# Kernel optimization log

Measured on AMD Instinct MI355X. Metric: run time of the kernel, lower is better.

The kernel has to match this reference:

```python
import jax, jax.numpy as jnp
import numpy as np
import math

B_, CIN, CH, COUT, H_, W_ = 4, 96, 96, 96, 48, 48
DSTATE, DTRANK = 16, math.ceil(CH / 16)
DI = 2 * CH


def conv2d(x, w, b=None, groups=1):
    # x: NCHW, w: OIHW, 'same' padding for odd kernels
    p = (w.shape[-1] - 1) // 2
    y = jax.lax.conv_general_dilated(x, w, (1, 1), [(p, p), (p, p)],
                                     dimension_numbers=('NCHW', 'OIHW', 'NCHW'),
                                     feature_group_count=groups)
    return y if b is None else y + b[None, :, None, None]


def layernorm_last(x, g, b, eps=1e-5):
    mu = x.mean(-1, keepdims=True)
    v = jnp.mean((x - mu) ** 2, -1, keepdims=True)
    return (x - mu) * jax.lax.rsqrt(v + eps) * g + b


def selective_scan(u, delta, A, Bs, Cs, D):
    # u, delta: (B,K,Di,L); A: (K,Di,N); Bs, Cs: (B,K,N,L); D: (K,Di)
    dt = jnp.moveaxis(delta, -1, 0)  # (L,B,K,Di)
    ut = jnp.moveaxis(u, -1, 0)
    Bt = jnp.moveaxis(Bs, -1, 0)     # (L,B,K,N)
    Ct = jnp.moveaxis(Cs, -1, 0)
    N = A.shape[-1]

    def step(h, inp):
        d, uu, bb, cc = inp
        # h: (B,K,Di,N)
        h = h * jnp.exp(d[..., None] * A) + (d * uu)[..., None] * bb[:, :, None, :]
        y = jnp.einsum('bkdn,bkn->bkd', h, cc)
        return h, y

    step = jax.checkpoint(step)
    h0 = jnp.zeros(u.shape[:3] + (N,), u.dtype)
    _, ys = jax.lax.scan(step, h0, (dt, ut, Bt, Ct))
    return jnp.moveaxis(ys, 0, -1) + u * D[None, :, :, None]


def ss2d(x, in_w, cw, cb, xpw, dtw, dtb, A_log, Dp, ong, onb, ow):
    # x: (B,H,W,C) -> (B,H,W,C)
    B, H, W, C = x.shape
    Di = in_w.shape[0] // 2
    xi, z = jnp.split(x @ in_w.T, 2, -1)
    xc = jax.nn.silu(conv2d(jnp.transpose(xi, (0, 3, 1, 2)), cw, cb, groups=Di))
    L = H * W
    xf = xc.reshape(B, Di, L)
    xwh = jnp.transpose(xc, (0, 1, 3, 2)).reshape(B, Di, L)
    xh = jnp.stack([xf, xwh], 1)                      # (B,2,Di,L)
    xs = jnp.concatenate([xh, jnp.flip(xh, -1)], 1)   # (B,4,Di,L) 4-direction cross-scan
    xdbl = jnp.einsum('bkdl,kcd->bkcl', xs, xpw)
    R = dtw.shape[-1]
    N = A_log.shape[-1]
    dts, Bs, Cs = jnp.split(xdbl, [R, R + N], axis=2)
    delta = jax.nn.softplus(jnp.einsum('bkrl,kdr->bkdl', dts, dtw) + dtb[None, :, :, None])
    A = -jnp.exp(A_log.reshape(4, Di, N))
    oy = selective_scan(xs, delta, A, Bs, Cs, Dp.reshape(4, Di))  # (B,4,Di,L)
    inv = jnp.flip(oy[:, 2:4], -1)
    why = jnp.transpose(oy[:, 1].reshape(B, Di, W, H), (0, 1, 3, 2)).reshape(B, Di, L)
    invwhy = jnp.transpose(inv[:, 1].reshape(B, Di, W, H), (0, 1, 3, 2)).reshape(B, Di, L)
    y = oy[:, 0] + inv[:, 0] + why + invwhy           # (B,Di,L)
    y = layernorm_last(jnp.transpose(y, (0, 2, 1)).reshape(B, H, W, Di), ong, onb)
    return (y * jax.nn.silu(z)) @ ow.T


def crm(x, s1, s2, gw, gb, p1, p2):
    C = x.shape[1]
    uc = C // 2
    up = conv2d(x[:, :uc], s1)
    low = conv2d(x[:, uc:], s2)
    Y1 = conv2d(up, gw, gb, groups=2) + conv2d(up, p1)
    Y2 = jnp.concatenate([conv2d(low, p2), low], 1)
    out = jnp.concatenate([Y1, Y2], 1)                # (B,2C,H,W)
    out = jax.nn.softmax(out.mean((2, 3), keepdims=True), axis=1) * out
    o1, o2 = jnp.split(out, 2, 1)
    return o1 + o2


def _forward(x, conv1_w, conv1_b, bn_g, bn_b, lin_w, lin_b, dw1_w, dw1_b, dw2_w, dw2_b, ag1_w, ag1_b, ag2_w, ag2_b, ln_g, ln_b, sq1_w, sq2_w, gwc_w, gwc_b, pwc1_w, pwc2_w, fin_w, fin_b, ss_in_w, ss_conv_w, ss_conv_b, ss_xproj_w, ss_dt_w, ss_dt_b, ss_Alog, ss_D, ss_outn_g, ss_outn_b, ss_out_w):
    C = conv1_w.shape[0]
    # conv1x1 + BatchNorm(eval: running mean 0, var 1) + ReLU
    h = conv2d(x, conv1_w, conv1_b)
    h = jax.nn.relu(h * (bn_g * jax.lax.rsqrt(jnp.float32(1.0 + 1e-5)))[None, :, None, None] + bn_b[None, :, None, None])
    # token-wise linear over channels
    t = jnp.transpose(h, (0, 2, 3, 1)) @ lin_w.T + lin_b
    h = jnp.transpose(t, (0, 3, 1, 2))
    # branch 1: DWConv -> SiLU -> SS2D
    x1 = jax.nn.silu(conv2d(h, dw1_w, dw1_b, groups=C))
    x1 = ss2d(jnp.transpose(x1, (0, 2, 3, 1)), ss_in_w, ss_conv_w, ss_conv_b,
              ss_xproj_w, ss_dt_w, ss_dt_b, ss_Alog, ss_D, ss_outn_g, ss_outn_b, ss_out_w)
    x1 = jnp.transpose(x1, (0, 3, 1, 2))
    # branch 2: DWConv -> SiLU -> AttentionGate modulation
    x2 = jax.nn.silu(conv2d(h, dw2_w, dw2_b, groups=C))
    g = jax.nn.sigmoid(conv2d(jax.nn.relu(conv2d(x2, ag1_w, ag1_b)), ag2_w, ag2_b))
    y = x1 + x2 * g
    # per-pixel channel LayerNorm
    mu = y.mean(1, keepdims=True)
    v = jnp.mean((y - mu) ** 2, 1, keepdims=True)
    y = (y - mu) * jax.lax.rsqrt(v + 1e-5) * ln_g[None, :, None, None] + ln_b[None, :, None, None]
    y = crm(y, sq1_w, sq2_w, gwc_w, gwc_b, pwc1_w, pwc2_w)
    out = jnp.transpose(y, (0, 2, 3, 1)) @ fin_w.T + fin_b
    return jnp.transpose(out, (0, 3, 1, 2))


def setup_inputs():
    key = jax.random.key(0)

    def rnd(i, shape, s=0.02):
        return (jax.random.normal(jax.random.fold_in(key, i), shape) * s).astype(jnp.float32)

    CH2, N, R = CH // 2, DSTATE, DTRANK
    inp = dict(
        x=jax.random.normal(jax.random.fold_in(key, 0), (B_, CIN, H_, W_), jnp.float32),
        conv1_w=rnd(1, (CH, CIN, 1, 1)), conv1_b=jnp.zeros((CH,), jnp.float32),
        bn_g=jnp.ones((CH,), jnp.float32), bn_b=jnp.zeros((CH,), jnp.float32),
        lin_w=rnd(2, (CH, CH)), lin_b=jnp.zeros((CH,), jnp.float32),
        dw1_w=rnd(3, (CH, 1, 3, 3)), dw1_b=jnp.zeros((CH,), jnp.float32),
        dw2_w=rnd(4, (CH, 1, 3, 3)), dw2_b=jnp.zeros((CH,), jnp.float32),
        ag1_w=rnd(5, (CH2, CH, 1, 1)), ag1_b=jnp.zeros((CH2,), jnp.float32),
        ag2_w=rnd(6, (CH, CH2, 1, 1)), ag2_b=jnp.zeros((CH,), jnp.float32),
        ln_g=jnp.ones((CH,), jnp.float32), ln_b=jnp.zeros((CH,), jnp.float32),
        sq1_w=rnd(7, (CH // 4, CH2, 1, 1)), sq2_w=rnd(8, (CH // 4, CH2, 1, 1)),
        gwc_w=rnd(9, (CH, CH // 8, 3, 3)), gwc_b=jnp.zeros((CH,), jnp.float32),
        pwc1_w=rnd(10, (CH, CH // 4, 1, 1)), pwc2_w=rnd(11, (CH - CH // 4, CH // 4, 1, 1)),
        fin_w=rnd(12, (COUT, CH)), fin_b=jnp.zeros((COUT,), jnp.float32),
        ss_in_w=rnd(13, (2 * DI, CH)),
        ss_conv_w=rnd(14, (DI, 1, 3, 3)), ss_conv_b=jnp.zeros((DI,), jnp.float32),
        ss_xproj_w=rnd(15, (4, R + 2 * N, DI)),
        ss_dt_w=rnd(16, (4, DI, R), R ** -0.5),
    )
    dt = jnp.exp(jax.random.uniform(jax.random.fold_in(key, 17), (4, DI)) *
                 (math.log(0.1) - math.log(0.001)) + math.log(0.001))
    inp['ss_dt_b'] = (dt + jnp.log(-jnp.expm1(-dt))).astype(jnp.float32)
    inp['ss_Alog'] = jnp.tile(jnp.log(jnp.arange(1, DSTATE + 1, dtype=jnp.float32))[None, :], (4 * DI, 1))
    inp['ss_D'] = jnp.ones((4 * DI,), jnp.float32)
    inp['ss_outn_g'] = jnp.ones((DI,), jnp.float32)
    inp['ss_outn_b'] = jnp.zeros((DI,), jnp.float32)
    inp['ss_out_w'] = rnd(18, (CH, DI))
    return inp


def reference(x, conv1_w, conv1_b, bn_g, bn_b, lin_w, lin_b, dw1_w, dw1_b, dw2_w, dw2_b, ag1_w, ag1_b, ag2_w, ag2_b, ln_g, ln_b, sq1_w, sq2_w, gwc_w, gwc_b, pwc1_w, pwc2_w, fin_w, fin_b, ss_in_w, ss_conv_w, ss_conv_b, ss_xproj_w, ss_dt_w, ss_dt_b, ss_Alog, ss_D, ss_outn_g, ss_outn_b, ss_out_w):
    return _forward(x, conv1_w, conv1_b, bn_g, bn_b, lin_w, lin_b, dw1_w, dw1_b, dw2_w, dw2_b, ag1_w, ag1_b, ag2_w, ag2_b, ln_g, ln_b, sq1_w, sq2_w, gwc_w, gwc_b, pwc1_w, pwc2_w, fin_w, fin_b, ss_in_w, ss_conv_w, ss_conv_b, ss_xproj_w, ss_dt_w, ss_dt_b, ss_Alog, ss_D, ss_outn_g, ss_outn_b, ss_out_w)
```

## Files before the change

### kernel.cpp

```cpp
#include <hip/hip_runtime.h>
#include <hip/hip_bf16.h>

#define Bn   4
#define CHn  96
#define Hh   48
#define Ww   48
#define Ll   2304
#define Pp   9216
#define DIn  192
#define Nn   16
#define Rr   6
#define Sseg   32
#define SEGL   72
#define NCH     9
#define HSPLIT 884736

__device__ inline float siluf(float x){ return x / (1.0f + __expf(-x)); }
__device__ inline float sigmf(float x){ return 1.0f / (1.0f + __expf(-x)); }

__device__ inline int pix_of(int k, int l){
  if (k == 0) return l;
  if (k == 1) return (l % 48) * 48 + l / 48;
  if (k == 2) return Ll - 1 - l;
  int lr = Ll - 1 - l; return (lr % 48) * 48 + lr / 48;
}
__device__ inline int l_of(int k, int p){
  if (k == 0) return p;
  if (k == 1) return (p % 48) * 48 + p / 48;
  if (k == 2) return Ll - 1 - p;
  return Ll - 1 - ((p % 48) * 48 + p / 48);
}

__device__ inline float4* hptr(float* lo, float* hi, size_t idx){
  return (float4*)(idx < HSPLIT ? lo + idx : hi + (idx - HSPLIT));
}

struct TArgs {
  const float* s[14];
  float* d[14];
  int rows[14];
  int cols[14];
};
__global__ void k_tr(TArgs a){
  int id = blockIdx.y;
  int n = a.rows[id] * a.cols[id];
  int t = blockIdx.x * blockDim.x + threadIdx.x;
  if (t < n){
    int r = t / a.cols[id];
    int c = t - r * a.cols[id];
    a.d[id][c * a.rows[id] + r] = a.s[id][t];
  }
}

__global__ void k_trx(const float* __restrict__ src, float* __restrict__ dst){
  __shared__ float tile[32][33];
  int pt = blockIdx.x, ct = blockIdx.y, b = blockIdx.z;
  int tx = threadIdx.x & 31, ty = threadIdx.x >> 5;
  #pragma unroll
  for (int i = 0; i < 4; ++i){
    int r = ty + i * 8;
    tile[r][tx] = src[((size_t)(b * CHn + ct * 32 + r)) * Ll + pt * 32 + tx];
  }
  __syncthreads();
  #pragma unroll
  for (int i = 0; i < 4; ++i){
    int r = ty + i * 8;
    dst[((size_t)(b * Ll + pt * 32 + r)) * CHn + ct * 32 + tx] = tile[tx][r];
  }
}

__global__ void k_tro(const float* __restrict__ src, float* __restrict__ dst){
  __shared__ float tile[32][33];
  int pt = blockIdx.x, ct = blockIdx.y, b = blockIdx.z;
  int tx = threadIdx.x & 31, ty = threadIdx.x >> 5;
  #pragma unroll
  for (int i = 0; i < 4; ++i){
    int r = ty + i * 8;
    tile[r][tx] = src[((size_t)(b * Ll + pt * 32 + r)) * CHn + ct * 32 + tx];
  }
  __syncthreads();
  #pragma unroll
  for (int i = 0; i < 4; ++i){
    int r = ty + i * 8;
    dst[((size_t)(b * CHn + ct * 32 + r)) * Ll + pt * 32 + tx] = tile[tx][r];
  }
}

__global__ void k_pre(const float* __restrict__ xT, const float* __restrict__ w1T, const float* __restrict__ b1,
                      const float* __restrict__ bng, const float* __restrict__ bnb,
                      const float* __restrict__ linT, const float* __restrict__ lb,
                      float* __restrict__ hlin){
  int p = blockIdx.x;
  int c = threadIdx.x;
  __shared__ float xv[CHn];
  __shared__ float hv[CHn];
  xv[c] = xT[(size_t)p * CHn + c];
  __syncthreads();
  float acc = 0.f;
  for (int i = 0; i < CHn; ++i) acc = fmaf(w1T[i * CHn + c], xv[i], acc);
  float s = bng[c] * rsqrtf(1.0f + 1e-5f);
  float h = fmaxf((acc + b1[c]) * s + bnb[c], 0.f);
  hv[c] = h;
  __syncthreads();
  float a2 = lb[c];
  for (int i = 0; i < CHn; ++i) a2 = fmaf(linT[i * CHn + c], hv[i], a2);
  hlin[(size_t)p * CHn + c] = a2;
}

__global__ void k_dw(const float* __restrict__ hlin,
                     const float* __restrict__ dw1w, const float* __restrict__ dw1b,
                     const float* __restrict__ dw2w, const float* __restrict__ dw2b,
                     float* __restrict__ x1pre, float* __restrict__ x2){
  int t = blockIdx.x * 256 + threadIdx.x;
  if (t >= Pp * CHn) return;
  int c = t % CHn; int p = t / CHn; int b = p / Ll; int pp = p - b * Ll;
  int r = pp / Ww; int cx = pp - r * Ww;
  float a1 = dw1b[c], a2 = dw2b[c];
  for (int dy = -1; dy <= 1; ++dy){
    int ny = r + dy; if ((unsigned)ny >= Hh) continue;
    for (int dx = -1; dx <= 1; ++dx){
      int nx = cx + dx; if ((unsigned)nx >= Ww) continue;
      float v = hlin[(size_t)((b * Ll) + ny * Ww + nx) * CHn + c];
      int wi = c * 9 + (dy + 1) * 3 + (dx + 1);
      a1 = fmaf(dw1w[wi], v, a1);
      a2 = fmaf(dw2w[wi], v, a2);
    }
  }
  x1pre[t] = siluf(a1);
  x2[t]   = siluf(a2);
}

__global__ void k_gate(const float* __restrict__ x2,
                       const float* __restrict__ ag1T, const float* __restrict__ ag1b,
                       const float* __restrict__ ag2T, const float* __restrict__ ag2b,
                       float* __restrict__ x2g){
  int p = blockIdx.x; int c = threadIdx.x;
  __shared__ float xv[CHn];
  __shared__ float rv[48];
  xv[c] = x2[(size_t)p * CHn + c];
  __syncthreads();
  if (c < 48){
    float a = ag1b[c];
    for (int i = 0; i < CHn; ++i) a = fmaf(ag1T[i * 48 + c], xv[i], a);
    rv[c] = fmaxf(a, 0.f);
  }
  __syncthreads();
  float a2 = ag2b[c];
  for (int tt = 0; tt < 48; ++tt) a2 = fmaf(ag2T[tt * CHn + c], rv[tt], a2);
  x2g[(size_t)p * CHn + c] = xv[c] * sigmf(a2);
}

__global__ __launch_bounds__(256) void k_ssin(const float* __restrict__ x1pre, const float* __restrict__ inT,
                                              float* __restrict__ xi, float* __restrict__ z){
  __shared__ float Xs[32][17];
  __shared__ float Wsh[32][128];
  int tid = threadIdx.x;
  int mt = blockIdx.x % 576; int nt = blockIdx.x / 576;
  int p0 = mt * 16, n0 = nt * 128;
  int tx = tid & 15, ty = tid >> 4;
  float acc[8];
  #pragma unroll
  for (int j = 0; j < 8; ++j) acc[j] = 0.f;
  for (int kc = 0; kc < 96; kc += 32){
    #pragma unroll
    for (int it = 0; it < 2; ++it){
      int e = it * 256 + tid; int dd = e & 31; int m = e >> 5;
      Xs[dd][m] = x1pre[(size_t)(p0 + m) * CHn + kc + dd];
    }
    #pragma unroll
    for (int it = 0; it < 16; ++it){
      int e = it * 256 + tid; int n = e & 127; int dd = e >> 7;
      Wsh[dd][n] = inT[(size_t)(kc + dd) * 384 + n0 + n];
    }
    __syncthreads();
    #pragma unroll
    for (int dd = 0; dd < 32; ++dd){
      float xv = Xs[dd][ty];
      #pragma unroll
      for (int j = 0; j < 8; ++j)
        acc[j] = fmaf(xv, Wsh[dd][tx + 16 * j], acc[j]);
    }
    __syncthreads();
  }
  int p = p0 + ty;
  #pragma unroll
  for (int j = 0; j < 8; ++j){
    int n = n0 + tx + 16 * j;
    float v = acc[j];
    if (n < 192) xi[(size_t)p * DIn + n] = v;
    else         z [(size_t)p * DIn + (n - 192)] = v;
  }
}

__global__ void k_ssdw(const float* __restrict__ xi, const float* __restrict__ scw,
                       const float* __restrict__ scb, float* __restrict__ xc){
  int t = blockIdx.x * 256 + threadIdx.x;
  if (t >= Pp * DIn) return;
  int d = t % DIn; int p = t / DIn; int b = p / Ll; int pp = p - b * Ll;
  int r = pp / Ww; int cx = pp - r * Ww;
  float a = scb[d];
  for (int dy = -1; dy <= 1; ++dy){
    int ny = r + dy; if ((unsigned)ny >= Hh) continue;
    for (int dx = -1; dx <= 1; ++dx){
      int nx = cx + dx; if ((unsigned)nx >= Ww) continue;
      float v = xi[(size_t)((b * Ll) + ny * Ww + nx) * DIn + d];
      a = fmaf(scw[d * 9 + (dy + 1) * 3 + (dx + 1)], v, a);
    }
  }
  xc[t] = siluf(a);
}

__global__ __launch_bounds__(256) void k_xproj(const float* __restrict__ xc,
    const float* __restrict__ xpwT, float* __restrict__ part){
  __shared__ float Xs[32][17];
  __shared__ float Wsh[32][160];
  int tid = threadIdx.x;
  int mt = blockIdx.x / 6; int kc = (blockIdx.x - mt * 6) * 32;
  int p0g = mt * 16;
  int tx = tid & 15, ty = tid >> 4;
  const float* xbase = xc + (size_t)p0g * DIn + kc;
  #pragma unroll
  for (int it = 0; it < 2; ++it){
    int e = it * 256 + tid; int dd = e & 31; int m = e >> 5;
    Xs[dd][m] = xbase[(size_t)m * DIn + dd];
  }
  #pragma unroll
  for (int it = 0; it < 20; ++it){
    int e = it * 256 + tid; int dd = e / 160; int n = e - dd * 160;
    Wsh[dd][n] = (n < 152) ? xpwT[(size_t)(kc + dd) * 152 + n] : 0.f;
  }
  __syncthreads();
  float acc[10];
  #pragma unroll
  for (int j = 0; j < 10; ++j) acc[j] = 0.f;
  #pragma unroll
  for (int dd = 0; dd < 32; ++dd){
    float xv = Xs[dd][ty];
    #pragma unroll
    for (int j = 0; j < 10; ++j)
      acc[j] = fmaf(xv, Wsh[dd][tx + 16 * j], acc[j]);
  }
  float* pb = part + ((size_t)blockIdx.x * 16 + ty) * 152;
  #pragma unroll
  for (int j = 0; j < 10; ++j){
    int n = tx + 16 * j;
    if (n < 152) pb[n] = acc[j];
  }
}

__global__ void k_xred(const float* __restrict__ part, float* __restrict__ bc,
                       float* __restrict__ dtsG){
  int t = blockIdx.x * 256 + threadIdx.x;
  if (t >= Pp * 152) return;
  int p = t / 152, n = t - p * 152;
  int mt = p >> 4, m = p & 15;
  const float* pb = part + ((size_t)(mt * 6) * 16 + m) * 152 + n;
  float s = 0.f;
  #pragma unroll
  for (int kc = 0; kc < 6; ++kc) s += pb[(size_t)kc * 16 * 152];
  int b = p / Ll; int pp = p - b * Ll;
  int k = n / 38, jj = n - k * 38;
  int l = l_of(k, pp);
  if (jj < 6) dtsG[((size_t)((b * 4 + k) * Ll + l)) * 6 + jj] = s;
  else        bc [((size_t)((b * 4 + k) * Ll + l)) * 32 + (jj - 6)] = s;
}

__global__ void k_pack(const float* __restrict__ dtsG, const float* __restrict__ dtwT,
                       const float* __restrict__ dtb, const float* __restrict__ xc,
                       float* __restrict__ packed){
  int t = blockIdx.x * 256 + threadIdx.x;
  if (t >= 36864 * DIn) return;
  int d = t % DIn; int row = t / DIn;
  int bk = row / Ll; int l = row - bk * Ll;
  int k = bk & 3; int b = bk >> 2;
  const float* ds = dtsG + (size_t)row * 6;
  float a = dtb[k * DIn + d];
  #pragma unroll
  for (int r = 0; r < 6; ++r)
    a = fmaf(dtwT[r * 768 + k * DIn + d], ds[r], a);
  float dt = fmaxf(a, 0.f) + __logf(1.0f + __expf(-fabsf(a)));
  int pix = pix_of(k, l);
  float u = xc[((size_t)(b * Ll) + pix) * DIn + d];
  int unit = bk * 12 + (d >> 4);
  size_t base = ((size_t)unit * Ll + l) * 32 + (d & 15);
  packed[base]      = dt;
  packed[base + 16] = dt * u;
}


__global__ __launch_bounds__(64) void k_scanA(const float* __restrict__ packed, const float* __restrict__ bc,
                                              const float* __restrict__ Alog,
                                              float* __restrict__ hend, float* __restrict__ dtsum){
  int blk = blockIdx.x; int unit = blk >> 5; int seg = blk & 31;
  int g = unit % 12; int bk = unit / 12; int k = bk & 3;
  int lane = threadIdx.x; int ch = lane >> 2; int ns = lane & 3; int nb = ns * 4;
  int d = g * 16 + ch;
  const int arow = (k * DIn + d) * 16 + nb;
  float A0 = -__expf(Alog[arow + 0]);
  float A1 = -__expf(Alog[arow + 1]);
  float A2 = -__expf(Alog[arow + 2]);
  float A3 = -__expf(Alog[arow + 3]);
  float h0 = 0.f, h1 = 0.f, h2 = 0.f, h3 = 0.f, dacc = 0.f;

  const int l0 = seg * SEGL;
  const float* pbase = packed + ((size_t)unit * Ll + l0) * 32;
  const float* bbase = bc + ((size_t)(bk * Ll) + l0) * 32;

  __shared__ float pl[256];
  __shared__ float blA[128];

  float4 pn = *(const float4*)(pbase + lane * 4);
  float4 bn;
  if (lane < 32) bn = *(const float4*)(bbase + (size_t)(lane >> 2) * 32 + (lane & 3) * 4);
  *(float4*)&pl[lane * 4] = pn;
  if (lane < 32) *(float4*)&blA[lane * 4] = bn;
  __syncthreads();

  for (int cc = 0; cc < NCH; ++cc){
    bool more = (cc + 1 < NCH);
    if (more){
      pn = *(const float4*)(pbase + (cc + 1) * 256 + lane * 4);
      if (lane < 32) bn = *(const float4*)(bbase + (size_t)((cc + 1) * 8 + (lane >> 2)) * 32 + (lane & 3) * 4);
    }
    #pragma unroll
    for (int lp = 0; lp < 8; ++lp){
      float dt = pl[lp * 32 + ch];
      float du = pl[lp * 32 + 16 + ch];
      float4 Bv = *(const float4*)&blA[lp * 16 + nb];
      dacc += dt;
      h0 = fmaf(h0, __expf(dt * A0), du * Bv.x);
      h1 = fmaf(h1, __expf(dt * A1), du * Bv.y);
      h2 = fmaf(h2, __expf(dt * A2), du * Bv.z);
      h3 = fmaf(h3, __expf(dt * A3), du * Bv.w);
    }
    __syncthreads();
    if (more){
      *(float4*)&pl[lane * 4] = pn;
      if (lane < 32) *(float4*)&blA[lane * 4] = bn;
    }
    __syncthreads();
  }
  size_t sb = (size_t)unit * Sseg + seg;
  *(float4*)&hend[sb * 256 + lane * 4] = make_float4(h0, h1, h2, h3);
  if (ns == 0) dtsum[sb * 16 + ch] = dacc;
}

__global__ __launch_bounds__(64) void k_comb(const float* __restrict__ Alog, const float* __restrict__ hend,
                                             const float* __restrict__ dtsum,
                                             float* __restrict__ hlo, float* __restrict__ hhi){
  int unit = blockIdx.x; int g = unit % 12; int bk = unit / 12; int k = bk & 3;
  int lane = threadIdx.x; int ch = lane >> 2; int ns = lane & 3; int nb = ns * 4;
  int d = g * 16 + ch;
  const int arow = (k * DIn + d) * 16 + nb;
  float A0 = -__expf(Alog[arow + 0]);
  float A1 = -__expf(Alog[arow + 1]);
  float A2 = -__expf(Alog[arow + 2]);
  float A3 = -__expf(Alog[arow + 3]);
  float h0 = 0.f, h1 = 0.f, h2 = 0.f, h3 = 0.f;
  for (int s = 0; s < Sseg; ++s){
    size_t sb = (size_t)unit * Sseg + s;
    *hptr(hlo, hhi, sb * 256 + lane * 4) = make_float4(h0, h1, h2, h3);
    float dsv = dtsum[sb * 16 + ch];
    float4 he = *(const float4*)&hend[sb * 256 + lane * 4];
    h0 = fmaf(h0, __expf(A0 * dsv), he.x);
    h1 = fmaf(h1, __expf(A1 * dsv), he.y);
    h2 = fmaf(h2, __expf(A2 * dsv), he.z);
    h3 = fmaf(h3, __expf(A3 * dsv), he.w);
  }
}

__global__ __launch_bounds__(64) void k_scanB(const float* __restrict__ packed, const float* __restrict__ bc,
                                              const float* __restrict__ Alog,
                                              float* __restrict__ hlo, float* __restrict__ hhi,
                                              float* __restrict__ ysum){
  int blk = blockIdx.x; int unit = blk >> 5; int seg = blk & 31;
  int g = unit % 12; int bk = unit / 12; int k = bk & 3; int b = bk >> 2;
  int lane = threadIdx.x; int ch = lane >> 2; int ns = lane & 3; int nb = ns * 4;
  int d = g * 16 + ch;
  const int arow = (k * DIn + d) * 16 + nb;
  float A0 = -__expf(Alog[arow + 0]);
  float A1 = -__expf(Alog[arow + 1]);
  float A2 = -__expf(Alog[arow + 2]);
  float A3 = -__expf(Alog[arow + 3]);
  size_t sb = (size_t)unit * Sseg + seg;
  float4 hi = *hptr(hlo, hhi, sb * 256 + lane * 4);
  float h0 = hi.x, h1 = hi.y, h2 = hi.z, h3 = hi.w;

  const int l0 = seg * SEGL;
  const float* pbase = packed + ((size_t)unit * Ll + l0) * 32;
  const float* bbase = bc + ((size_t)(bk * Ll) + l0) * 32;
  float* ybase = ysum + (size_t)(b * Ll) * DIn + d;

  __shared__ float pl[256];
  __shared__ float bl[256];

  float4 pn = *(const float4*)(pbase + lane * 4);
  float4 bn = *(const float4*)(bbase + lane * 4);
  *(float4*)&pl[lane * 4] = pn;
  *(float4*)&bl[lane * 4] = bn;
  __syncthreads();

  for (int cc = 0; cc < NCH; ++cc){
    bool more = (cc + 1 < NCH);
    if (more){
      pn = *(const float4*)(pbase + (cc + 1) * 256 + lane * 4);
      bn = *(const float4*)(bbase + (cc + 1) * 256 + lane * 4);
    }
    #pragma unroll
    for (int lp = 0; lp < 8; ++lp){
      float dt = pl[lp * 32 + ch];
      float du = pl[lp * 32 + 16 + ch];
      float4 Bv = *(const float4*)&bl[lp * 32 + nb];
      float4 Cv = *(const float4*)&bl[lp * 32 + 16 + nb];
      h0 = fmaf(h0, __expf(dt * A0), du * Bv.x);
      h1 = fmaf(h1, __expf(dt * A1), du * Bv.y);
      h2 = fmaf(h2, __expf(dt * A2), du * Bv.z);
      h3 = fmaf(h3, __expf(dt * A3), du * Bv.w);
      float yp = fmaf(h0, Cv.x, fmaf(h1, Cv.y, fmaf(h2, Cv.z, h3 * Cv.w)));
      yp += __shfl_xor(yp, 1);
      yp += __shfl_xor(yp, 2);
      if (ns == 0){
        int l = l0 + cc * 8 + lp;
        int pix = pix_of(k, l);
        atomicAdd(ybase + (size_t)pix * DIn, yp);
      }
    }
    __syncthreads();
    if (more){
      *(float4*)&pl[lane * 4] = pn;
      *(float4*)&bl[lane * 4] = bn;
    }
    __syncthreads();
  }
}

__device__ inline float block_sum_192(float* red, int d, float v){
  red[d] = v; __syncthreads();
  if (d < 96) red[d] += red[d + 96]; __syncthreads();
  if (d < 48) red[d] += red[d + 48]; __syncthreads();
  if (d < 24) red[d] += red[d + 24]; __syncthreads();
  if (d < 12) red[d] += red[d + 12]; __syncthreads();
  if (d < 6)  red[d] += red[d + 6];  __syncthreads();
  float tot = red[0] + red[1] + red[2] + red[3] + red[4] + red[5];
  __syncthreads();
  return tot;
}
__device__ inline float block_sum_96(float* red, int d, float v){
  if (d < 96) red[d] = v; __syncthreads();
  if (d < 48) red[d] += red[d + 48]; __syncthreads();
  if (d < 24) red[d] += red[d + 24]; __syncthreads();
  if (d < 12) red[d] += red[d + 12]; __syncthreads();
  if (d < 6)  red[d] += red[d + 6];  __syncthreads();
  float tot = red[0] + red[1] + red[2] + red[3] + red[4] + red[5];
  __syncthreads();
  return tot;
}

__global__ void k_combine(const float* __restrict__ ysum, const float* __restrict__ xc,
                          const float* __restrict__ z, const float* __restrict__ Dp,
                          const float* __restrict__ ong, const float* __restrict__ onb,
                          const float* __restrict__ owT, const float* __restrict__ x2g,
                          const float* __restrict__ lng, const float* __restrict__ lnb,
                          const float* __restrict__ sq1T, const float* __restrict__ sq2T,
                          float* __restrict__ ul){
  int p = blockIdx.x;
  int d = threadIdx.x;
  __shared__ float red[192];
  __shared__ float ygv[192];
  __shared__ float crs[96];
  float yv = ysum[(size_t)p * DIn + d];
  float u = xc[(size_t)p * DIn + d];
  float Ds = Dp[d] + Dp[192 + d] + Dp[384 + d] + Dp[576 + d];
  yv = fmaf(u, Ds, yv);
  float mu = block_sum_192(red, d, yv) * (1.f / 192.f);
  float dv = yv - mu;
  float var = block_sum_192(red, d, dv * dv) * (1.f / 192.f);
  float yn = dv * rsqrtf(var + 1e-5f) * ong[d] + onb[d];
  float zv = z[(size_t)p * DIn + d];
  ygv[d] = yn * (zv * sigmf(zv));
  __syncthreads();
  float sval = 0.f;
  if (d < 96){
    float acc = 0.f;
    for (int dd = 0; dd < 192; ++dd) acc = fmaf(owT[dd * 96 + d], ygv[dd], acc);
    sval = acc + x2g[(size_t)p * CHn + d];
  }
  float mu2 = block_sum_96(red, d, sval) * (1.f / 96.f);
  float dv2 = sval - mu2;
  float var2 = block_sum_96(red, d, (d < 96) ? dv2 * dv2 : 0.f) * (1.f / 96.f);
  if (d < 96) crs[d] = dv2 * rsqrtf(var2 + 1e-5f) * lng[d] + lnb[d];
  __syncthreads();
  if (d < 48){
    float a = 0.f;
    if (d < 24){
      for (int i = 0; i < 48; ++i) a = fmaf(sq1T[i * 24 + d], crs[i], a);
    } else {
      int o = d - 24;
      for (int i = 0; i < 48; ++i) a = fmaf(sq2T[i * 24 + o], crs[48 + i], a);
    }
    ul[(size_t)p * 48 + d] = a;
  }
}

__global__ void k_y(const float* __restrict__ ul, const float* __restrict__ gwcT,
                    const float* __restrict__ gwcb, const float* __restrict__ pwc1T,
                    const float* __restrict__ pwc2T, float* __restrict__ Ybig){
  int p = blockIdx.x; int b = p / Ll; int pp = p - b * Ll;
  int r = pp / Ww; int cx = pp - r * Ww;
  int oc = threadIdx.x;
  __shared__ float ulv[48];
  if (oc < 48) ulv[oc] = ul[(size_t)p * 48 + oc];
  __syncthreads();
  float acc;
  if (oc < 96){
    acc = gwcb[oc];
    int grp = oc / 48;
    for (int dy = -1; dy <= 1; ++dy){
      int ny = r + dy; if ((unsigned)ny >= Hh) continue;
      for (int dx = -1; dx <= 1; ++dx){
        int nx = cx + dx; if ((unsigned)nx >= Ww) continue;
        const float* un = ul + (size_t)((b * Ll) + ny * Ww + nx) * 48 + grp * 12;
        int k9 = (dy + 1) * 3 + (dx + 1);
        #pragma unroll
        for (int i = 0; i < 12; ++i) acc = fmaf(gwcT[(i * 9 + k9) * 96 + oc], un[i], acc);
      }
    }
    for (int i = 0; i < 24; ++i) acc = fmaf(pwc1T[i * 96 + oc], ulv[i], acc);
  } else if (oc < 168){
    int o2 = oc - 96; acc = 0.f;
    for (int i = 0; i < 24; ++i) acc = fmaf(pwc2T[i * 72 + o2], ulv[24 + i], acc);
  } else {
    acc = ulv[24 + oc - 168];
  }
  Ybig[(size_t)p * 192 + oc] = acc;
}

__global__ void k_csum(const float* __restrict__ Ybig, float* __restrict__ csum_p){
  int b = blockIdx.x / 36; int ch = blockIdx.x - b * 36;
  int t = threadIdx.x;
  if (t >= 192) return;
  float acc = 0.f;
  const float* base = Ybig + (size_t)(b * Ll + ch * 64) * 192 + t;
  #pragma unroll 4
  for (int i = 0; i < 64; ++i) acc += base[(size_t)i * 192];
  csum_p[(size_t)blockIdx.x * 192 + t] = acc;
}

__global__ void k_softmax(const float* __restrict__ csum_p, float* __restrict__ wsm){
  int b = blockIdx.x; int t = threadIdx.x;
  __shared__ float red[192];
  float m = 0.f;
  for (int cc = 0; cc < 36; ++cc) m += csum_p[(size_t)(b * 36 + cc) * 192 + t];
  m *= (1.f / 2304.f);
  red[t] = m; __syncthreads();
  if (t < 96) red[t] = fmaxf(red[t], red[t + 96]); __syncthreads();
  if (t < 48) red[t] = fmaxf(red[t], red[t + 48]); __syncthreads();
  if (t < 24) red[t] = fmaxf(red[t], red[t + 24]); __syncthreads();
  if (t < 12) red[t] = fmaxf(red[t], red[t + 12]); __syncthreads();
  if (t < 6)  red[t] = fmaxf(red[t], red[t + 6]);  __syncthreads();
  float mx = fmaxf(fmaxf(fmaxf(red[0], red[1]), fmaxf(red[2], red[3])), fmaxf(red[4], red[5]));
  __syncthreads();
  float e = __expf(m - mx);
  float s = block_sum_192(red, t, e);
  wsm[b * 192 + t] = e / s;
}

__global__ void k_final(const float* __restrict__ Ybig, const float* __restrict__ wsm,
                        const float* __restrict__ finT, const float* __restrict__ finb,
                        float* __restrict__ outT){
  int p = blockIdx.x; int b = p / Ll;
  int c = threadIdx.x;
  __shared__ float ov[96];
  float o = wsm[b * 192 + c]      * Ybig[(size_t)p * 192 + c]
          + wsm[b * 192 + 96 + c] * Ybig[(size_t)p * 192 + 96 + c];
  ov[c] = o; __syncthreads();
  float acc = finb[c];
  for (int i = 0; i < 96; ++i) acc = fmaf(finT[i * 96 + c], ov[i], acc);
  outT[(size_t)p * CHn + c] = acc;
}

extern "C" void kernel_launch(void* const* d_in, const int* in_sizes, int n_in,
                              void* d_out, int out_size, void* d_ws, size_t ws_size,
                              hipStream_t stream) {
  const float* x     = (const float*)d_in[0];
  const float* w1    = (const float*)d_in[1];
  const float* b1    = (const float*)d_in[2];
  const float* bng   = (const float*)d_in[3];
  const float* bnb   = (const float*)d_in[4];
  const float* linw  = (const float*)d_in[5];
  const float* linb  = (const float*)d_in[6];
  const float* dw1w  = (const float*)d_in[7];
  const float* dw1b  = (const float*)d_in[8];
  const float* dw2w  = (const float*)d_in[9];
  const float* dw2b  = (const float*)d_in[10];
  const float* ag1w  = (const float*)d_in[11];
  const float* ag1b  = (const float*)d_in[12];
  const float* ag2w  = (const float*)d_in[13];
  const float* ag2b  = (const float*)d_in[14];
  const float* lng   = (const float*)d_in[15];
  const float* lnb   = (const float*)d_in[16];
  const float* sq1w  = (const float*)d_in[17];
  const float* sq2w  = (const float*)d_in[18];
  const float* gwcw  = (const float*)d_in[19];
  const float* gwcb  = (const float*)d_in[20];
  const float* pwc1w = (const float*)d_in[21];
  const float* pwc2w = (const float*)d_in[22];
  const float* finw  = (const float*)d_in[23];
  const float* finb  = (const float*)d_in[24];
  const float* inw   = (const float*)d_in[25];
  const float* scw   = (const float*)d_in[26];
  const float* scb   = (const float*)d_in[27];
  const float* xpw   = (const float*)d_in[28];
  const float* dtw   = (const float*)d_in[29];
  const float* dtb   = (const float*)d_in[30];
  const float* Alog  = (const float*)d_in[31];
  const float* Dp    = (const float*)d_in[32];
  const float* ong   = (const float*)d_in[33];
  const float* onb   = (const float*)d_in[34];
  const float* oww   = (const float*)d_in[35];

  float* ws = (float*)d_ws;
  float* hlin   = ws + 0;
  float* dtsum  = ws + 442368;
  float* x1pre  = ws + 884736;
  float* x2     = ws + 1769472;
  float* x2g    = ws + 2654208;
  float* xibuf  = ws + 3538944;
  float* zbuf   = ws + 5308416;
  float* xcbuf  = ws + 7077888;
  float* packed = ws + 8847360;
  float* bcbuf  = ws + 23003136;
  float* ysum   = ws + 24182784;
  float* wT     = ws + 25952256;

  float* dtsG    = x2;
  float* hend    = xibuf;
  float* hinitlo = x1pre;
  float* hinithi = x2;
  float* ulb     = hlin;
  float* Ybig    = xibuf;
  float* csum_p  = x1pre;
  float* wsmb    = x1pre + 27648;
  float* xT      = packed;
  float* part    = packed;
  float* outT    = packed;

  float* w1T   = wT + 0;
  float* linT  = wT + 9216;
  float* ag1T  = wT + 18432;
  float* ag2T  = wT + 23040;
  float* inT   = wT + 27648;
  float* owT   = wT + 64512;
  float* pwc1T = wT + 82944;
  float* pwc2T = wT + 85248;
  float* finT  = wT + 86976;
  float* sq1T  = wT + 96192;
  float* sq2T  = wT + 97344;
  float* gwcT  = wT + 98496;
  float* dtwT  = wT + 108864;
  float* xpwT  = wT + 113472;

  TArgs ta;
  const float* srcs[14] = {w1, linw, ag1w, ag2w, inw, oww, pwc1w, pwc2w, finw, sq1w, sq2w, gwcw, dtw, xpw};
  float* dsts[14]       = {w1T, linT, ag1T, ag2T, inT, owT, pwc1T, pwc2T, finT, sq1T, sq2T, gwcT, dtwT, xpwT};
  int rows[14] = {96, 96, 48, 96, 384, 96, 96, 72, 96, 24, 24, 96, 768, 152};
  int cols[14] = {96, 96, 96, 48, 96, 192, 24, 24, 96, 48, 48, 108, 6, 192};
  for (int i = 0; i < 14; ++i){ ta.s[i] = srcs[i]; ta.d[i] = dsts[i]; ta.rows[i] = rows[i]; ta.cols[i] = cols[i]; }

  k_tr<<<dim3(144, 14), 256, 0, stream>>>(ta);
  k_trx<<<dim3(72, 3, 4), 256, 0, stream>>>(x, xT);
  k_pre<<<Pp, CHn, 0, stream>>>(xT, w1T, b1, bng, bnb, linT, linb, hlin);
  k_dw<<<(Pp * CHn) / 256, 256, 0, stream>>>(hlin, dw1w, dw1b, dw2w, dw2b, x1pre, x2);
  k_gate<<<Pp, CHn, 0, stream>>>(x2, ag1T, ag1b, ag2T, ag2b, x2g);
  k_ssin<<<576 * 3, 256, 0, stream>>>(x1pre, inT, xibuf, zbuf);
  k_ssdw<<<(Pp * DIn) / 256, 256, 0, stream>>>(xibuf, scw, scb, xcbuf);
  k_xproj<<<576 * 6, 256, 0, stream>>>(xcbuf, xpwT, part);
  k_xred<<<(Pp * 152 + 255) / 256, 256, 0, stream>>>(part, bcbuf, dtsG);
  k_pack<<<(36864 * DIn) / 256, 256, 0, stream>>>(dtsG, dtwT, dtb, xcbuf, packed);
  hipMemsetAsync(ysum, 0, (size_t)1769472 * 4, stream);
  k_scanA<<<192 * Sseg, 64, 0, stream>>>(packed, bcbuf, Alog, hend, dtsum);
  k_comb<<<192, 64, 0, stream>>>(Alog, hend, dtsum, hinitlo, hinithi);
  k_scanB<<<192 * Sseg, 64, 0, stream>>>(packed, bcbuf, Alog, hinitlo, hinithi, ysum);
  k_combine<<<Pp, DIn, 0, stream>>>(ysum, xcbuf, zbuf, Dp, ong, onb, owT, x2g, lng, lnb, sq1T, sq2T, ulb);
  k_y<<<Pp, 192, 0, stream>>>(ulb, gwcT, gwcb, pwc1T, pwc2T, Ybig);
  k_csum<<<144, 256, 0, stream>>>(Ybig, csum_p);
  k_softmax<<<4, 192, 0, stream>>>(csum_p, wsmb);
  k_final<<<Pp, CHn, 0, stream>>>(Ybig, wsmb, finT, finb, outT);
  k_tro<<<dim3(72, 3, 4), 256, 0, stream>>>(outT, (float*)d_out);
}
```

Measured before the change: 356.5 us.

## Restructure k_combine to process 16 pixels per block with shuffle reductions

Rewrites the post-scan combine kernel so each 256-thread block handles 16 pixels, with 16 lanes per pixel. The two layernorms use sub-wavefront shuffle reductions instead of shared-memory tree reductions with many barriers. Each lane now computes 6 output channels of the 192->96 projection and 3 of the squeeze outputs, so every loaded weight is reused across channels. This targets barrier overhead and the poor lane utilisation of the 192-thread-per-pixel layout. In exchange each thread holds more registers, and weight loads are now strided across lanes.

```diff
diff --git a/kernel.cpp b/kernel.cpp
--- a/kernel.cpp
+++ b/kernel.cpp
@@ -445,60 +445,96 @@
   __syncthreads();
   return tot;
 }
-__device__ inline float block_sum_96(float* red, int d, float v){
-  if (d < 96) red[d] = v; __syncthreads();
-  if (d < 48) red[d] += red[d + 48]; __syncthreads();
-  if (d < 24) red[d] += red[d + 24]; __syncthreads();
-  if (d < 12) red[d] += red[d + 12]; __syncthreads();
-  if (d < 6)  red[d] += red[d + 6];  __syncthreads();
-  float tot = red[0] + red[1] + red[2] + red[3] + red[4] + red[5];
-  __syncthreads();
-  return tot;
-}
-
-__global__ void k_combine(const float* __restrict__ ysum, const float* __restrict__ xc,
+
+__global__ __launch_bounds__(256) void k_combine(const float* __restrict__ ysum, const float* __restrict__ xc,
                           const float* __restrict__ z, const float* __restrict__ Dp,
                           const float* __restrict__ ong, const float* __restrict__ onb,
                           const float* __restrict__ owT, const float* __restrict__ x2g,
                           const float* __restrict__ lng, const float* __restrict__ lnb,
                           const float* __restrict__ sq1T, const float* __restrict__ sq2T,
                           float* __restrict__ ul){
-  int p = blockIdx.x;
-  int d = threadIdx.x;
-  __shared__ float red[192];
-  __shared__ float ygv[192];
-  __shared__ float crs[96];
-  float yv = ysum[(size_t)p * DIn + d];
-  float u = xc[(size_t)p * DIn + d];
-  float Ds = Dp[d] + Dp[192 + d] + Dp[384 + d] + Dp[576 + d];
-  yv = fmaf(u, Ds, yv);
-  float mu = block_sum_192(red, d, yv) * (1.f / 192.f);
-  float dv = yv - mu;
-  float var = block_sum_192(red, d, dv * dv) * (1.f / 192.f);
-  float yn = dv * rsqrtf(var + 1e-5f) * ong[d] + onb[d];
-  float zv = z[(size_t)p * DIn + d];
-  ygv[d] = yn * (zv * sigmf(zv));
-  __syncthreads();
-  float sval = 0.f;
-  if (d < 96){
-    float acc = 0.f;
-    for (int dd = 0; dd < 192; ++dd) acc = fmaf(owT[dd * 96 + d], ygv[dd], acc);
-    sval = acc + x2g[(size_t)p * CHn + d];
-  }
-  float mu2 = block_sum_96(red, d, sval) * (1.f / 96.f);
-  float dv2 = sval - mu2;
-  float var2 = block_sum_96(red, d, (d < 96) ? dv2 * dv2 : 0.f) * (1.f / 96.f);
-  if (d < 96) crs[d] = dv2 * rsqrtf(var2 + 1e-5f) * lng[d] + lnb[d];
-  __syncthreads();
-  if (d < 48){
+  __shared__ float ygs[16 * 200];
+  __shared__ float crs_s[16 * 104];
+  int tid = threadIdx.x;
+  int m = tid >> 4, t = tid & 15;
+  int p = blockIdx.x * 16 + m;
+  const float* yrow = ysum + (size_t)p * DIn;
+  const float* urow = xc   + (size_t)p * DIn;
+  const float* zrow = z    + (size_t)p * DIn;
+
+  float yv[12];
+  float s1 = 0.f;
+  #pragma unroll
+  for (int j = 0; j < 12; ++j){
+    int d = t + 16 * j;
+    float Ds = Dp[d] + Dp[192 + d] + Dp[384 + d] + Dp[576 + d];
+    float v = fmaf(urow[d], Ds, yrow[d]);
+    yv[j] = v; s1 += v;
+  }
+  #pragma unroll
+  for (int mk = 1; mk < 16; mk <<= 1) s1 += __shfl_xor(s1, mk, 16);
+  float mu = s1 * (1.f / 192.f);
+  float s2 = 0.f;
+  #pragma unroll
+  for (int j = 0; j < 12; ++j){ float dv = yv[j] - mu; s2 += dv * dv; }
+  #pragma unroll
+  for (int mk = 1; mk < 16; mk <<= 1) s2 += __shfl_xor(s2, mk, 16);
+  float rstd = rsqrtf(s2 * (1.f / 192.f) + 1e-5f);
+  #pragma unroll
+  for (int j = 0; j < 12; ++j){
+    int d = t + 16 * j;
+    float yn = (yv[j] - mu) * rstd * ong[d] + onb[d];
+    float zv = zrow[d];
+    ygs[m * 200 + d] = yn * (zv * sigmf(zv));
+  }
+  __syncthreads();
+
+  float acc[6];
+  #pragma unroll
+  for (int jj = 0; jj < 6; ++jj) acc[jj] = 0.f;
+  const float* yg = &ygs[m * 200];
+  for (int dd = 0; dd < 192; ++dd){
+    float xv = yg[dd];
+    const float* wrow = owT + dd * 96 + t;
+    #pragma unroll
+    for (int jj = 0; jj < 6; ++jj)
+      acc[jj] = fmaf(xv, wrow[16 * jj], acc[jj]);
+  }
+  float sv[6]; float s3 = 0.f;
+  #pragma unroll
+  for (int jj = 0; jj < 6; ++jj){
+    int c = t + 16 * jj;
+    sv[jj] = acc[jj] + x2g[(size_t)p * CHn + c];
+    s3 += sv[jj];
+  }
+  #pragma unroll
+  for (int mk = 1; mk < 16; mk <<= 1) s3 += __shfl_xor(s3, mk, 16);
+  float mu2 = s3 * (1.f / 96.f);
+  float s4 = 0.f;
+  #pragma unroll
+  for (int jj = 0; jj < 6; ++jj){ float dv = sv[jj] - mu2; s4 += dv * dv; }
+  #pragma unroll
+  for (int mk = 1; mk < 16; mk <<= 1) s4 += __shfl_xor(s4, mk, 16);
+  float rstd2 = rsqrtf(s4 * (1.f / 96.f) + 1e-5f);
+  #pragma unroll
+  for (int jj = 0; jj < 6; ++jj){
+    int c = t + 16 * jj;
+    crs_s[m * 104 + c] = (sv[jj] - mu2) * rstd2 * lng[c] + lnb[c];
+  }
+  __syncthreads();
+
+  const float* cr = &crs_s[m * 104];
+  #pragma unroll
+  for (int jj = 0; jj < 3; ++jj){
+    int o = t + 16 * jj;
     float a = 0.f;
-    if (d < 24){
-      for (int i = 0; i < 48; ++i) a = fmaf(sq1T[i * 24 + d], crs[i], a);
+    if (o < 24){
+      for (int i = 0; i < 48; ++i) a = fmaf(sq1T[i * 24 + o], cr[i], a);
     } else {
-      int o = d - 24;
-      for (int i = 0; i < 48; ++i) a = fmaf(sq2T[i * 24 + o], crs[48 + i], a);
-    }
-    ul[(size_t)p * 48 + d] = a;
+      int oo = o - 24;
+      for (int i = 0; i < 48; ++i) a = fmaf(sq2T[i * 24 + oo], cr[48 + i], a);
+    }
+    ul[(size_t)p * 48 + o] = a;
   }
 }
 
@@ -681,7 +717,7 @@
   k_scanA<<<192 * Sseg, 64, 0, stream>>>(packed, bcbuf, Alog, hend, dtsum);
   k_comb<<<192, 64, 0, stream>>>(Alog, hend, dtsum, hinitlo, hinithi);
   k_scanB<<<192 * Sseg, 64, 0, stream>>>(packed, bcbuf, Alog, hinitlo, hinithi, ysum);
-  k_combine<<<Pp, DIn, 0, stream>>>(ysum, xcbuf, zbuf, Dp, ong, onb, owT, x2g, lng, lnb, sq1T, sq2T, ulb);
+  k_combine<<<576, 256, 0, stream>>>(ysum, xcbuf, zbuf, Dp, ong, onb, owT, x2g, lng, lnb, sq1T, sq2T, ulb);
   k_y<<<Pp, 192, 0, stream>>>(ulb, gwcT, gwcb, pwc1T, pwc2T, Ybig);
   k_csum<<<144, 256, 0, stream>>>(Ybig, csum_p);
   k_softmax<<<4, 192, 0, stream>>>(csum_p, wsmb);
```

New measurement: 349.9 us. No clear change (-1.9%).
